# Performance work log

Measured on AMD Instinct MI355X. Metric: run time of the kernel, lower is better.

The kernel has to match this reference:

```python
import jax, jax.numpy as jnp
import numpy as np

B, TX, TY, C, H = 16, 256, 2048, 80, 256
NEG = -1e9


def setup_inputs() -> dict:
    key = jax.random.key(0)
    k = jax.random.split(key, 6)
    en = jax.random.normal(k[0], (B, H, TX), jnp.float32)           # encoder out [B,H,Tx]
    mu = jax.random.normal(k[1], (B, C, TX), jnp.float32)           # MDN means [B,C,Tx]
    log_sigma = 0.1 * jax.random.normal(k[2], (B, C, TX), jnp.float32)
    y = jax.random.normal(k[3], (B, TY, C), jnp.float32)            # mel target [B,Ty,C]
    # lengths near max so y_len >= x_len (monotonic path exists)
    x_lengths = TX - jax.random.randint(k[4], (B,), 0, 64, dtype=jnp.int32)
    y_lengths = TY - jax.random.randint(k[5], (B,), 0, 512, dtype=jnp.int32)
    return {"en": en, "mu": mu, "log_sigma": log_sigma, "y": y,
            "x_lengths": x_lengths, "y_lengths": y_lengths}


def compute_log_probs(mu, log_sigma, y):
    """logp[b,x,t] = -0.5*mean_c[(y[b,t,c]-mu[b,x,c])^2/sigma^2] - 0.5*mean_c[log_sigma].
    Expanded as y^2 - 2*y*mu + mu^2 to avoid materializing [B,Tx,Ty,C]."""
    mu_t = jnp.swapaxes(mu, 1, 2)          # [B,Tx,C]
    ls_t = jnp.swapaxes(log_sigma, 1, 2)   # [B,Tx,C]
    inv_var = jnp.exp(-2.0 * ls_t)         # 1/sigma^2
    t1 = jnp.einsum('byc,bxc->bxy', y * y, inv_var)
    t2 = jnp.einsum('byc,bxc->bxy', y, mu_t * inv_var)
    t3 = jnp.sum(mu_t * mu_t * inv_var, axis=-1)[..., None]
    expo = -0.5 * (t1 - 2.0 * t2 + t3) / C
    return expo - 0.5 * jnp.mean(ls_t, axis=-1, keepdims=True)  # [B,Tx,Ty]


def _mas_single(logp, x_len, y_len):
    """Viterbi monotonic alignment search for one batch item. logp: [Tx,Ty]."""
    tx, ty = logp.shape
    ii = jnp.arange(tx)
    row_ok = ii < x_len

    def fwd(v_prev, col):
        shifted = jnp.concatenate([jnp.full((1,), NEG, v_prev.dtype), v_prev[:-1]])
        diag = shifted > v_prev                      # came from i-1
        v = jnp.maximum(v_prev, shifted) + col
        v = jnp.where(row_ok, v, NEG)
        return v, diag

    v0 = jnp.where(ii == 0, 0.0, NEG).astype(logp.dtype)
    _, diag = jax.lax.scan(fwd, v0, jnp.swapaxes(logp, 0, 1))  # diag: [Ty,Tx] bool

    def bwd(idx, inp):
        d_j, j = inp
        active = j < y_len
        row = jnp.where(active, (ii == idx).astype(logp.dtype), 0.0)
        new_idx = jnp.where(active, idx - d_j[idx].astype(idx.dtype), idx)
        new_idx = jnp.maximum(new_idx, 0)
        return new_idx, row

    idx0 = (x_len - 1).astype(jnp.int32)
    _, rows = jax.lax.scan(bwd, idx0, (diag, jnp.arange(ty)), reverse=True)
    return jnp.swapaxes(rows, 0, 1)  # path [Tx,Ty]


def maximum_path(logp, x_lengths, y_lengths):
    return jax.vmap(_mas_single)(logp, x_lengths, y_lengths)


def generate_path(dr, x_mask, y_mask):
    """Durations [B,Tx] -> hard alignment [B,Tx,Ty]."""
    cum = jnp.cumsum(dr, axis=-1)                                  # [B,Tx]
    j = jnp.arange(y_mask.shape[-1], dtype=dr.dtype)
    m = (j[None, None, :] < cum[:, :, None]).astype(dr.dtype)      # [B,Tx,Ty]
    path = m - jnp.concatenate([jnp.zeros_like(m[:, :1]), m[:, :-1]], axis=1)
    return path * (x_mask[:, :, None] * y_mask[:, None, :])


def reference(en, mu, log_sigma, y, x_lengths, y_lengths):
    x_mask = (jnp.arange(TX)[None, :] < x_lengths[:, None]).astype(en.dtype)
    y_mask = (jnp.arange(TY)[None, :] < y_lengths[:, None]).astype(en.dtype)
    logp = compute_log_probs(mu, log_sigma, y)                     # [B,Tx,Ty]
    attn_mas = jax.lax.stop_gradient(maximum_path(logp, x_lengths, y_lengths))
    dr_mas = jnp.sum(attn_mas, axis=-1)                            # [B,Tx]
    attn = generate_path(dr_mas, x_mask, y_mask)                   # [B,Tx,Ty]
    o_en_ex = jnp.einsum('bxy,bcx->bcy', attn, en)                 # [B,H,Ty]
    return (o_en_ex, attn, dr_mas, logp)
```

## Files before the change

### kernel.cpp

```cpp
#include <hip/hip_runtime.h>
#include <hip/hip_bf16.h>
#include <cstdint>
#include <cstddef>

#define B_ 16
#define TX_ 256
#define TY_ 2048
#define C_ 80
#define H_ 256
#define NEG_ -1e9f
#define NEG_I (int)0xCE6E6B28
#define CHUNK_ 32
#define NCHUNK_ (TY_ / CHUNK_)

#define GLD16(gp, lp) __builtin_amdgcn_global_load_lds( \
    (const __attribute__((address_space(1))) unsigned int*)(gp), \
    (__attribute__((address_space(3))) unsigned int*)(lp), 16, 0, 0)

#define BT_STEP(JB)                                                           \
    {                                                                         \
        unsigned bit = ((unsigned)(W >> (((ii & 4) << 3) | ((JB) << 2)        \
                                         | (ii & 3))) & 1u)                   \
                     & (unsigned)(ii > 0);                                    \
        ii -= (int)bit;                                                       \
        W = (bit && ((ii & 7) == 7)) ? Wl : W;                                \
    }

__global__ __launch_bounds__(256) void logp_kernel(
    const float* __restrict__ mu, const float* __restrict__ ls,
    const float* __restrict__ y, float* __restrict__ logp_out,
    float* __restrict__ logp_t)
{
    __shared__ float2 coef[16 * 80];
    __shared__ float  aux[16 * 80];
    __shared__ float  Kx[16];
    __shared__ float  yt[16 * 1028];

    const int tid = threadIdx.x;
    const int t0 = blockIdx.x * 1024;
    const int x0 = blockIdx.y * 16;
    const int b  = blockIdx.z;

    for (int i = tid; i < 16 * 80; i += 256) {
        int c = i >> 4, x = i & 15;
        float m = mu[(size_t)(b * C_ + c) * TX_ + x0 + x];
        float l = ls[(size_t)(b * C_ + c) * TX_ + x0 + x];
        float w = __expf(-2.f * l);
        coef[x * 80 + c] = make_float2(w, -2.f * m * w);
        aux[x * 80 + c]  = fmaf(m * m, w, l);
    }
    __syncthreads();
    if (tid < 16) {
        float s = 0.f;
        for (int c = 0; c < C_; ++c) s += aux[tid * 80 + c];
        Kx[tid] = -0.5f * s / (float)C_;
    }

    float acc[16][4];
#pragma unroll
    for (int x = 0; x < 16; ++x)
#pragma unroll
        for (int r = 0; r < 4; ++r) acc[x][r] = 0.f;

    const float4* y4 = (const float4*)y;
    for (int c0 = 0; c0 < C_; c0 += 16) {
        __syncthreads();
        for (int it = 0; it < 16; ++it) {
            int f = tid + it * 256;
            int t = f >> 2, k = f & 3;
            float4 v = y4[(size_t)(b * TY_ + t0 + t) * 20 + (c0 >> 2) + k];
            yt[(4 * k + 0) * 1028 + t] = v.x;
            yt[(4 * k + 1) * 1028 + t] = v.y;
            yt[(4 * k + 2) * 1028 + t] = v.z;
            yt[(4 * k + 3) * 1028 + t] = v.w;
        }
        __syncthreads();
        for (int cl = 0; cl < 16; ++cl) {
            const float4 yv = *reinterpret_cast<const float4*>(&yt[cl * 1028 + 4 * tid]);
            float4 y2 = make_float4(yv.x * yv.x, yv.y * yv.y, yv.z * yv.z, yv.w * yv.w);
#pragma unroll
            for (int x = 0; x < 16; ++x) {
                float2 f2 = coef[x * 80 + c0 + cl];
                acc[x][0] = fmaf(y2.x, f2.x, fmaf(yv.x, f2.y, acc[x][0]));
                acc[x][1] = fmaf(y2.y, f2.x, fmaf(yv.y, f2.y, acc[x][1]));
                acc[x][2] = fmaf(y2.z, f2.x, fmaf(yv.z, f2.y, acc[x][2]));
                acc[x][3] = fmaf(y2.w, f2.x, fmaf(yv.w, f2.y, acc[x][3]));
            }
        }
    }

#pragma unroll
    for (int x = 0; x < 16; ++x) {
        float kx = Kx[x];
#pragma unroll
        for (int r = 0; r < 4; ++r) acc[x][r] = fmaf(acc[x][r], -0.5f / (float)C_, kx);
        float4 out = make_float4(acc[x][0], acc[x][1], acc[x][2], acc[x][3]);
        *reinterpret_cast<float4*>(
            &logp_out[(size_t)(b * TX_ + x0 + x) * TY_ + t0 + 4 * tid]) = out;
    }
#pragma unroll
    for (int r = 0; r < 4; ++r) {
#pragma unroll
        for (int q = 0; q < 4; ++q) {
            float4 out = make_float4(acc[4 * q + 0][r], acc[4 * q + 1][r],
                                     acc[4 * q + 2][r], acc[4 * q + 3][r]);
            *reinterpret_cast<float4*>(
                &logp_t[(size_t)(b * TY_ + t0 + 4 * tid + r) * TX_ + x0 + 4 * q]) = out;
        }
    }
}

__global__ __launch_bounds__(128) void mas_fwd_kernel(
    const float* __restrict__ logp_t, unsigned int* __restrict__ diag_g)
{
    __shared__ float ring[2][CHUNK_ * 256];
    const int tid = threadIdx.x;
    const int wave = tid >> 6;
    const int lane = tid & 63;
    const int b = blockIdx.x;

    const float* colbase = logp_t + (size_t)b * TY_ * TX_;
    unsigned int* diag = diag_g + (size_t)b * (TY_ / 8) * 64;

    float v0 = (lane == 0) ? 0.f : NEG_, v1 = NEG_, v2 = NEG_, v3 = NEG_;
    unsigned int accb = 0;

    if (wave == 1) {
        const float* src = colbase + lane * 4;
#pragma unroll
        for (int k = 0; k < CHUNK_; ++k)
            GLD16(src + k * 256, &ring[0][k * 256]);
    }
    __syncthreads();

    for (int n = 0; n < NCHUNK_; ++n) {
        if (wave == 1) {
            if (n + 1 < NCHUNK_) {
                const float* src = colbase + (size_t)(n + 1) * CHUNK_ * 256 + lane * 4;
                float* dst = &ring[(n + 1) & 1][0];
#pragma unroll
                for (int k = 0; k < CHUNK_; ++k)
                    GLD16(src + k * 256, dst + k * 256);
            }
        } else {
            const float* buf = &ring[n & 1][0];
#pragma unroll
            for (int k = 0; k < CHUNK_; ++k) {
                float4 c = *reinterpret_cast<const float4*>(&buf[k * 256 + lane * 4]);
                int shi = __builtin_amdgcn_update_dpp(
                    NEG_I, __float_as_int(v3), 0x138 , 0xF, 0xF, false);
                float sh0 = __int_as_float(shi);
                accb |= (sh0 > v0) ? (1u << ((k & 7) * 4)) : 0u;
                accb |= (v0 > v1) ? (2u << ((k & 7) * 4)) : 0u;
                accb |= (v1 > v2) ? (4u << ((k & 7) * 4)) : 0u;
                accb |= (v2 > v3) ? (8u << ((k & 7) * 4)) : 0u;
                float m0 = fmaxf(v0, sh0);
                float m1 = fmaxf(v1, v0);
                float m2 = fmaxf(v2, v1);
                float m3 = fmaxf(v3, v2);
                v0 = m0 + c.x; v1 = m1 + c.y; v2 = m2 + c.z; v3 = m3 + c.w;
                if ((k & 7) == 7) {
                    diag[(n * 4 + (k >> 3)) * 64 + lane] = accb;
                    accb = 0;
                }
            }
        }
        __syncthreads();
    }
}

__global__ __launch_bounds__(256) void mas_tab_kernel(
    const unsigned int* __restrict__ diag_g, unsigned char* __restrict__ E_g)
{
    const int t  = threadIdx.x;
    const int cg = blockIdx.x;
    const int b  = blockIdx.y;
    const unsigned int* dg = diag_g + (size_t)b * (TY_ / 8) * 64;
    unsigned char* Eb = E_g + (size_t)b * (TY_ / 8) * 256;
    const int p = t >> 3;

    for (int k = 0; k < 16; ++k) {
        const int c = cg * 16 + k;
        unsigned long long W  = *(const unsigned long long*)&dg[c * 64 + 2 * p];
        unsigned long long Wl = p > 0
            ? *(const unsigned long long*)&dg[c * 64 + 2 * (p - 1)] : 0ULL;
        int ii = t;
#pragma unroll
        for (int jb = 7; jb >= 0; --jb) BT_STEP(jb)
        Eb[c * 256 + t] = (unsigned char)ii;
    }
}

__global__ __launch_bounds__(256) void mas_bt_kernel(
    const unsigned int* __restrict__ diag_g, const unsigned char* __restrict__ E_g,
    const int* __restrict__ xlen, const int* __restrict__ ylen,
    float* __restrict__ dr_out, int* __restrict__ idx_out)
{
    __shared__ unsigned char E[256 * 256];
    __shared__ unsigned char entry_s[256];
    __shared__ int rows_l[TY_];
    __shared__ int cnt_l[TX_];
    const int tid = threadIdx.x;
    const int b = blockIdx.x;
    const int x_len = xlen[b];
    const int y_len = ylen[b];

    cnt_l[tid] = 0;

    const uint4* srcE = (const uint4*)(E_g + (size_t)b * (TY_ / 8) * 256);
    uint4* dstE = (uint4*)E;
#pragma unroll
    for (int it = 0; it < 16; ++it)
        dstE[tid + it * 256] = srcE[tid + it * 256];
    __syncthreads();

    const unsigned int* dg = diag_g + (size_t)b * (TY_ / 8) * 64;
    int* ib = idx_out + (size_t)b * TY_;
    const int jc = (y_len - 1) >> 3;

    if (tid == 0) {
        int ii = x_len - 1;
        int p = ii >> 3;
        unsigned long long W  = *(const unsigned long long*)&dg[jc * 64 + 2 * p];
        unsigned long long Wl = p > 0
            ? *(const unsigned long long*)&dg[jc * 64 + 2 * (p - 1)] : 0ULL;
        for (int jb = (y_len - 1) & 7; jb >= 0; --jb) {
            int j = 8 * jc + jb;
            ib[j] = ii; rows_l[j] = ii;
            BT_STEP(jb)
        }
        int cur = ii;
        for (int c = jc - 1; c >= 0; --c) {
            entry_s[c] = (unsigned char)cur;
            cur = E[c * 256 + cur];
        }
    }
    __syncthreads();

    if (tid < jc) {
        const int c = tid;
        int ii = entry_s[c];
        int p = ii >> 3;
        unsigned long long W  = *(const unsigned long long*)&dg[c * 64 + 2 * p];
        unsigned long long Wl = p > 0
            ? *(const unsigned long long*)&dg[c * 64 + 2 * (p - 1)] : 0ULL;
        int r[8];
#pragma unroll
        for (int jb = 7; jb >= 0; --jb) {
            r[jb] = ii;
            BT_STEP(jb)
        }
        *reinterpret_cast<int4*>(&ib[8 * c])     = make_int4(r[0], r[1], r[2], r[3]);
        *reinterpret_cast<int4*>(&ib[8 * c + 4]) = make_int4(r[4], r[5], r[6], r[7]);
        *reinterpret_cast<int4*>(&rows_l[8 * c])     = make_int4(r[0], r[1], r[2], r[3]);
        *reinterpret_cast<int4*>(&rows_l[8 * c + 4]) = make_int4(r[4], r[5], r[6], r[7]);
    }
    __syncthreads();

    for (int t = tid; t < TY_; t += 256)
        if (t < y_len) atomicAdd(&cnt_l[rows_l[t]], 1);
    __syncthreads();
    dr_out[(size_t)b * TX_ + tid] = (float)cnt_l[tid];
}

__global__ __launch_bounds__(256) void emit_kernel(
    const float* __restrict__ en, const int* __restrict__ ylen,
    const int* __restrict__ idx_in, float* __restrict__ o_en,
    float* __restrict__ attn)
{
    const int tid = threadIdx.x;
    const int b = blockIdx.x;
    const int r = blockIdx.y;
    const int y_len = ylen[b];
    const int* ib = idx_in + (size_t)b * TY_;

    if (r < 256) {
        const int x = r;
        float* out = attn + ((size_t)b * TX_ + x) * TY_;
        for (int t = tid; t < TY_; t += 256) {
            int ii = ib[t];
            out[t] = (t < y_len && ii == x) ? 1.f : 0.f;
        }
    } else {
        const int h = r - 256;
        __shared__ float enr[256];
        enr[tid] = en[((size_t)b * H_ + h) * TX_ + tid];
        __syncthreads();
        float* out = o_en + ((size_t)b * H_ + h) * TY_;
        for (int t = tid; t < TY_; t += 256) {
            int ii = ib[t];
            bool a = (t < y_len);
            int is = a ? ii : 0;
            out[t] = a ? enr[is] : 0.f;
        }
    }
}

extern "C" void kernel_launch(void* const* d_in, const int* in_sizes, int n_in,
                              void* d_out, int out_size, void* d_ws, size_t ws_size,
                              hipStream_t stream)
{
    const float* en = (const float*)d_in[0];
    const float* mu = (const float*)d_in[1];
    const float* ls = (const float*)d_in[2];
    const float* y  = (const float*)d_in[3];
    const int* xl   = (const int*)d_in[4];
    const int* yl   = (const int*)d_in[5];

    float* o_en = (float*)d_out;
    float* attn = o_en + (size_t)B_ * TX_ * TY_;
    float* dr   = attn + (size_t)B_ * TX_ * TY_;
    float* logp = dr + (size_t)B_ * TX_;

    float* logp_t = attn;
    unsigned int* diag_g = (unsigned int*)o_en;
    unsigned char* E_g = (unsigned char*)logp_t;
    int* idxArr = (int*)d_ws;

    dim3 g1(2, 16, 16);
    logp_kernel<<<g1, 256, 0, stream>>>(mu, ls, y, logp, logp_t);

    mas_fwd_kernel<<<dim3(16), dim3(128), 0, stream>>>(logp_t, diag_g);
    mas_tab_kernel<<<dim3(16, 16), dim3(256), 0, stream>>>(diag_g, E_g);
    mas_bt_kernel<<<dim3(16), dim3(256), 0, stream>>>(diag_g, E_g, xl, yl, dr, idxArr);

    dim3 g3(16, 512);
    emit_kernel<<<g3, 256, 0, stream>>>(en, yl, idxArr, o_en, attn);
}
```

Before: 321.2 us.

## Replace LDS double-buffered MAS forward with register prefetch and inline-asm bit packing

```diff
diff --git a/kernel.cpp b/kernel.cpp
--- a/kernel.cpp
+++ b/kernel.cpp
@@ -10,16 +10,11 @@
 #define H_ 256
 #define NEG_ -1e9f
 #define NEG_I (int)0xCE6E6B28
-#define CHUNK_ 32
-#define NCHUNK_ (TY_ / CHUNK_)
-
-#define GLD16(gp, lp) __builtin_amdgcn_global_load_lds( \
-    (const __attribute__((address_space(1))) unsigned int*)(gp), \
-    (__attribute__((address_space(3))) unsigned int*)(lp), 16, 0, 0)
 
 #define BT_STEP(JB)                                                           \
     {                                                                         \
-        unsigned bit = ((unsigned)(W >> (((ii & 4) << 3) | ((JB) << 2)        \
+        unsigned bit = ((unsigned)(W >> (((ii & 4) << 3)                      \
+                                         | ((7 - (JB)) << 2)                  \
                                          | (ii & 3))) & 1u)                   \
                      & (unsigned)(ii > 0);                                    \
         ii -= (int)bit;                                                       \
@@ -110,62 +105,69 @@
     }
 }
 
-__global__ __launch_bounds__(128) void mas_fwd_kernel(
+#define PD_ 32
+
+#define DP_STEP(CVAL, KC)                                                     \
+    {                                                                         \
+        int shi = __builtin_amdgcn_update_dpp(                                \
+            NEG_I, __float_as_int(v3), 0x138 , 0xF, 0xF, false); \
+        float sh0 = __int_as_float(shi);                                      \
+        asm("v_cmp_gt_f32 vcc, %5, %6\n\t"                                    \
+            "v_addc_co_u32 %0, vcc, %1, %1, vcc\n\t"                          \
+            "v_cmp_gt_f32 vcc, %4, %5\n\t"                                    \
+            "v_addc_co_u32 %0, vcc, %0, %0, vcc\n\t"                          \
+            "v_cmp_gt_f32 vcc, %3, %4\n\t"                                    \
+            "v_addc_co_u32 %0, vcc, %0, %0, vcc\n\t"                          \
+            "v_cmp_gt_f32 vcc, %2, %3\n\t"                                    \
+            "v_addc_co_u32 %0, vcc, %0, %0, vcc\n\t"                          \
+            : "=&v"(accb)                                                     \
+            : "v"(accb), "v"(sh0), "v"(v0), "v"(v1), "v"(v2), "v"(v3)         \
+            : "vcc");                                                         \
+        float m0 = fmaxf(v0, sh0);                                            \
+        float m1 = fmaxf(v1, v0);                                             \
+        float m2 = fmaxf(v2, v1);                                             \
+        float m3 = fmaxf(v3, v2);                                             \
+        v0 = m0 + (CVAL).x; v1 = m1 + (CVAL).y;                               \
+        v2 = m2 + (CVAL).z; v3 = m3 + (CVAL).w;                               \
+        if (((KC) & 7) == 7) {                                                \
+            diag[((KC) >> 3) * 64 + lane] = accb;                             \
+            accb = 0u;                                                        \
+        }                                                                     \
+    }
+
+__global__ __launch_bounds__(64, 1) void mas_fwd_kernel(
     const float* __restrict__ logp_t, unsigned int* __restrict__ diag_g)
 {
-    __shared__ float ring[2][CHUNK_ * 256];
-    const int tid = threadIdx.x;
-    const int wave = tid >> 6;
-    const int lane = tid & 63;
+    const int lane = threadIdx.x;
     const int b = blockIdx.x;
 
-    const float* colbase = logp_t + (size_t)b * TY_ * TX_;
+    const float* colp = logp_t + (size_t)b * TY_ * TX_ + lane * 4;
     unsigned int* diag = diag_g + (size_t)b * (TY_ / 8) * 64;
 
     float v0 = (lane == 0) ? 0.f : NEG_, v1 = NEG_, v2 = NEG_, v3 = NEG_;
     unsigned int accb = 0;
 
-    if (wave == 1) {
-        const float* src = colbase + lane * 4;
-#pragma unroll
-        for (int k = 0; k < CHUNK_; ++k)
-            GLD16(src + k * 256, &ring[0][k * 256]);
-    }
-    __syncthreads();
-
-    for (int n = 0; n < NCHUNK_; ++n) {
-        if (wave == 1) {
-            if (n + 1 < NCHUNK_) {
-                const float* src = colbase + (size_t)(n + 1) * CHUNK_ * 256 + lane * 4;
-                float* dst = &ring[(n + 1) & 1][0];
-#pragma unroll
-                for (int k = 0; k < CHUNK_; ++k)
-                    GLD16(src + k * 256, dst + k * 256);
-            }
-        } else {
-            const float* buf = &ring[n & 1][0];
-#pragma unroll
-            for (int k = 0; k < CHUNK_; ++k) {
-                float4 c = *reinterpret_cast<const float4*>(&buf[k * 256 + lane * 4]);
-                int shi = __builtin_amdgcn_update_dpp(
-                    NEG_I, __float_as_int(v3), 0x138 , 0xF, 0xF, false);
-                float sh0 = __int_as_float(shi);
-                accb |= (sh0 > v0) ? (1u << ((k & 7) * 4)) : 0u;
-                accb |= (v0 > v1) ? (2u << ((k & 7) * 4)) : 0u;
-                accb |= (v1 > v2) ? (4u << ((k & 7) * 4)) : 0u;
-                accb |= (v2 > v3) ? (8u << ((k & 7) * 4)) : 0u;
-                float m0 = fmaxf(v0, sh0);
-                float m1 = fmaxf(v1, v0);
-                float m2 = fmaxf(v2, v1);
-                float m3 = fmaxf(v3, v2);
-                v0 = m0 + c.x; v1 = m1 + c.y; v2 = m2 + c.z; v3 = m3 + c.w;
-                if ((k & 7) == 7) {
-                    diag[(n * 4 + (k >> 3)) * 64 + lane] = accb;
-                    accb = 0;
-                }
-            }
-        }
-        __syncthreads();
+    float4 pre[PD_];
+#pragma unroll
+    for (int j = 0; j < PD_; ++j)
+        pre[j] = *reinterpret_cast<const float4*>(colp + (size_t)j * 256);
+
+    for (int k0 = 0; k0 < TY_ - PD_; k0 += PD_) {
+        const float* nxt = colp + (size_t)(k0 + PD_) * 256;
+#pragma unroll
+        for (int j = 0; j < PD_; ++j) {
+            float4 c = pre[j];
+            pre[j] = *reinterpret_cast<const float4*>(nxt + (size_t)j * 256);
+            DP_STEP(c, k0 + j)
+        }
+    }
+    {
+        const int k0 = TY_ - PD_;
+#pragma unroll
+        for (int j = 0; j < PD_; ++j) {
+            float4 c = pre[j];
+            DP_STEP(c, k0 + j)
+        }
     }
 }
 
@@ -320,7 +322,7 @@
     dim3 g1(2, 16, 16);
     logp_kernel<<<g1, 256, 0, stream>>>(mu, ls, y, logp, logp_t);
 
-    mas_fwd_kernel<<<dim3(16), dim3(128), 0, stream>>>(logp_t, diag_g);
+    mas_fwd_kernel<<<dim3(16), dim3(64), 0, stream>>>(logp_t, diag_g);
     mas_tab_kernel<<<dim3(16, 16), dim3(256), 0, stream>>>(diag_g, E_g);
     mas_bt_kernel<<<dim3(16), dim3(256), 0, stream>>>(diag_g, E_g, xl, yl, dr, idxArr);
 
```

Measured after the change: 302.1 us. 5.9% less time.
